# Kernel tuning notes

Hardware: AMD Instinct MI355X
Metric: run time of the kernel (lower is better)

Reference implementation:

```python
import jax, jax.numpy as jnp
import numpy as np

B, H, W = 64, 512, 512
TOP_K = 200
N_OBJS = 200
KP_THRES = 0.1
IOU_THR = 0.5
RESIZE_H, RESIZE_W = 512.0, 512.0


def setup_inputs() -> dict:
    key = jax.random.key(0)
    k1, k2, k3 = jax.random.split(key, 3)
    heatmap_y = jax.random.uniform(k1, (B, H), dtype=jnp.float32)
    heatmap_x = jax.random.uniform(k2, (B, W), dtype=jnp.float32)
    # box sizes in heatmap pixels (scaled so boxes are non-degenerate)
    size_maps = jax.random.uniform(k3, (B, H, W, 2), dtype=jnp.float32) * 64.0
    origin_shapes = jnp.full((B, 2), 1024.0, dtype=jnp.float32)
    return {"heatmap_y": heatmap_y, "heatmap_x": heatmap_x,
            "size_maps": size_maps, "origin_shapes": origin_shapes}


def _iou_one_vs_all(box, boxes):
    # box: (4,) [y1,x1,y2,x2]; boxes: (N,4)
    yy1 = jnp.maximum(box[0], boxes[:, 0])
    xx1 = jnp.maximum(box[1], boxes[:, 1])
    yy2 = jnp.minimum(box[2], boxes[:, 2])
    xx2 = jnp.minimum(box[3], boxes[:, 3])
    inter = jnp.maximum(yy2 - yy1, 0.0) * jnp.maximum(xx2 - xx1, 0.0)
    a1 = (box[2] - box[0]) * (box[3] - box[1])
    a2 = (boxes[:, 2] - boxes[:, 0]) * (boxes[:, 3] - boxes[:, 1])
    denom = a1 + a2 - inter
    return jnp.where(denom > 0.0, inter / jnp.maximum(denom, 1e-12), 0.0)


def _nms_single(boxes, scores):
    # greedy NMS over N boxes, selecting up to N_OBJS (TF combined_non_max_suppression,
    # single class, clip_boxes=False, score_threshold=-inf, zero-padded output)
    N = boxes.shape[0]

    def body(i, st):
        active, sb, ss, cnt = st
        ms = jnp.where(active, scores, -jnp.inf)
        j = jnp.argmax(ms)
        valid = ms[j] > -jnp.inf
        bj = boxes[j]
        ious = _iou_one_vs_all(bj, boxes)
        active = active & (ious <= IOU_THR)
        active = active.at[j].set(False)
        sb = sb.at[i].set(jnp.where(valid, bj, jnp.zeros_like(bj)))
        ss = ss.at[i].set(jnp.where(valid, scores[j], 0.0))
        return (active, sb, ss, cnt + valid.astype(jnp.int32))

    init = (jnp.ones((N,), dtype=bool),
            jnp.zeros((N_OBJS, 4), boxes.dtype),
            jnp.zeros((N_OBJS,), scores.dtype),
            jnp.array(0, jnp.int32))
    _, sb, ss, cnt = jax.lax.fori_loop(0, N_OBJS, body, init)
    return sb, ss, cnt


def _decode(heatmap_y, heatmap_x, size_maps, origin_shapes):
    Bd, Hd = heatmap_y.shape
    Wd = heatmap_x.shape[1]
    # rank-1 heatmap: matmul(hy[...,None], hx[...,None]^T) == outer product -> (B,H,W)
    hm = heatmap_y[:, :, None] * heatmap_x[:, None, :]
    # 3x3 max-pool peak suppression (CenterNet keep-mask)
    hmax = jax.lax.reduce_window(hm, -jnp.inf, jax.lax.max,
                                 (1, 3, 3), (1, 1, 1), 'SAME')
    hm = jnp.where(hmax == hm, hm, 0.0)
    # top-k over flattened spatial dims (c == 1)
    scores, idx = jax.lax.top_k(hm.reshape(Bd, Hd * Wd), TOP_K)  # (B,K)
    ys = idx // Wd
    xs = idx % Wd
    bidx = jnp.arange(Bd)[:, None]
    sizes = size_maps[bidx, ys, xs]                      # (B,K,2) gather_nd
    centers = jnp.stack([ys, xs], axis=-1).astype(hm.dtype)  # (B,K,2)
    tls = jnp.maximum(centers - sizes / 2.0, 0.0)        # clamp tl at 0
    brs = centers + sizes / 2.0
    br_y = jnp.minimum(brs[..., 0], RESIZE_H - 1.0)
    br_x = jnp.minimum(brs[..., 1], RESIZE_W - 1.0)
    # resize back to original image coords
    ratio = origin_shapes / jnp.asarray([RESIZE_H, RESIZE_W], dtype=hm.dtype)  # (B,2)
    ry = ratio[:, 0:1]
    rx = ratio[:, 1:2]
    boxes = jnp.stack([tls[..., 0] * ry, tls[..., 1] * rx,
                       br_y * ry, br_x * rx], axis=-1)   # (B,K,4)
    # threshold mask + scatter into -1-initialized output (indices == own positions)
    mask = scores > KP_THRES
    boxes = jnp.where(mask[..., None], boxes, -1.0)
    sc = jnp.where(mask, scores, -1.0)
    if TOP_K < N_OBJS:
        boxes = jnp.pad(boxes, ((0, 0), (0, N_OBJS - TOP_K), (0, 0)), constant_values=-1.0)
        sc = jnp.pad(sc, ((0, 0), (0, N_OBJS - TOP_K)), constant_values=-1.0)
    nb, ns, _cnt = jax.vmap(_nms_single)(boxes, sc)      # (B,N_OBJS,4), (B,N_OBJS)
    # post: -1 boxes -> inf, 0 (NMS padding) boxes -> inf
    nb = jnp.where(nb == -1.0, jnp.inf, nb)
    nb = jnp.where(nb == 0.0, jnp.inf, nb)
    classes = jnp.zeros_like(ns)                         # single class -> class id 0
    out = jnp.concatenate([nb, ns[..., None], classes[..., None]], axis=-1)
    return out.reshape(-1, N_OBJS, 6)


def reference(heatmap_y, heatmap_x, size_maps, origin_shapes):
    return _decode(heatmap_y, heatmap_x, size_maps, origin_shapes)
```

## Files before the change

### kernel.cpp

```cpp
#include <hip/hip_runtime.h>
#include <stdint.h>

#define NT 1024
#define HW 512
#define TOPK 200
#define STAIR_GEN 256
#define STAIR_T 204
#define MAXCAND 1024
#define MAXCLOSE 320

typedef unsigned long long u64;
typedef unsigned u32;

__global__ __launch_bounds__(NT) void decode_nms_kernel(
    const float* __restrict__ hyg, const float* __restrict__ hxg,
    const float* __restrict__ size_maps, const float* __restrict__ origin,
    float* __restrict__ out)
{
#pragma clang fp contract(off)
  const int b = blockIdx.x;
  const int tid = threadIdx.x;

  __shared__ float hy[HW], hx[HW];
  __shared__ int   cyI[MAXCLOSE], cxI[MAXCLOSE];
  __shared__ float cyV[MAXCLOSE], cyM[MAXCLOSE], cxV[MAXCLOSE], cxM[MAXCLOSE];
  __shared__ u64   pK[2][HW];
  __shared__ float sV[2][HW];
  __shared__ int   sI[2][HW];
  __shared__ u64   cand[MAXCAND];
  __shared__ float tS[TOPK];
  __shared__ int   tL[TOPK];
  __shared__ float4 bb4[256];
  __shared__ u64   sup[256][4];
  __shared__ int   pickL[TOPK];
  __shared__ int   nCY, nCX, nPk0, nPk1, nCand, survSh;
  __shared__ u32   Tbits;

  if (tid == 0) { nCY = 0; nCX = 0; nPk0 = 0; nPk1 = 0; nCand = 0; Tbits = 0; }
  if (tid < HW) {
    hy[tid] = hyg[(size_t)b * HW + tid];
    hx[tid] = hxg[(size_t)b * HW + tid];
  }
  __syncthreads();

  if (tid < HW) {
    int i = tid;
    float v = hy[i], m = v;
    if (i > 0)      m = fmaxf(m, hy[i - 1]);
    if (i < HW - 1) m = fmaxf(m, hy[i + 1]);
    if (v >= m * (1.0f - 1e-6f)) {
      int p = atomicAdd(&nCY, 1);
      if (p < MAXCLOSE) { cyI[p] = i; cyV[p] = v; cyM[p] = m; }
    }
    if (v == m) {
      int p = atomicAdd(&nPk0, 1);
      pK[0][p] = ((u64)__float_as_uint(v) << 32) | (u64)(0xFFFFFFFFu - (u32)i);
    }
    float w = hx[i], mw = w;
    if (i > 0)      mw = fmaxf(mw, hx[i - 1]);
    if (i < HW - 1) mw = fmaxf(mw, hx[i + 1]);
    if (w >= mw * (1.0f - 1e-6f)) {
      int p = atomicAdd(&nCX, 1);
      if (p < MAXCLOSE) { cxI[p] = i; cxV[p] = w; cxM[p] = mw; }
    }
    if (w == mw) {
      int p = atomicAdd(&nPk1, 1);
      pK[1][p] = ((u64)__float_as_uint(w) << 32) | (u64)(0xFFFFFFFFu - (u32)i);
    }
  }
  __syncthreads();

  int NP0 = nPk0, NP1 = nPk1;
  for (int d = 0; d < 2; ++d) {
    int n = d ? NP1 : NP0;
    if (tid < n) {
      u64 key = pK[d][tid];
      int rank = 0;
      #pragma unroll 8
      for (int j = 0; j < n; ++j) rank += (pK[d][j] > key) ? 1 : 0;
      sV[d][rank] = __uint_as_float((u32)(key >> 32));
      sI[d][rank] = (int)(0xFFFFFFFFu - (u32)(key & 0xFFFFFFFFu));
    }
  }
  __syncthreads();

  {
    int a = tid + 1;
    if (a <= STAIR_T && a <= NP0) {
      int bn = (STAIR_T + a - 1) / a;
      if (bn <= NP1) atomicMax(&Tbits, __float_as_uint(sV[0][a - 1] * sV[1][bn - 1]));
    }
  }
  __syncthreads();
  const float T = __uint_as_float(Tbits);

  int ncy = nCY < MAXCLOSE ? nCY : MAXCLOSE;
  int ncx = nCX < MAXCLOSE ? nCX : MAXCLOSE;
  if (tid < ncy) {
    int yi = tid;
    float vy = cyV[yi], mvy = cyM[yi];
    bool py = (vy == mvy);
    int ybase = cyI[yi] * HW;
    #pragma unroll 8
    for (int xi = 0; xi < ncx; ++xi) {
      float vx = cxV[xi], mvx = cxM[xi];
      if (py && vx == mvx) continue;
      float p = vy * vx;
      if (p == mvy * mvx && p > 0.1f && p >= T) {
        int pos = atomicAdd(&nCand, 1);
        if (pos < MAXCAND)
          cand[pos] = ((u64)__float_as_uint(p) << 32)
                    | (u64)(0xFFFFFFFFu - (u32)(ybase + cxI[xi]));
      }
    }
  }

  {
    int NY = NP0 < STAIR_GEN ? NP0 : STAIR_GEN;
    {
      int i = tid >> 6, jc = tid & 63;
      if (i < NY) {
        int jmax = STAIR_GEN / (i + 1); if (jmax > NP1) jmax = NP1;
        int jlo = jc * 4, jhi = jlo + 4; if (jhi > jmax) jhi = jmax;
        float vy = sV[0][i]; int ybase = sI[0][i] * HW;
        #pragma unroll 4
        for (int j = jlo; j < jhi; ++j) {
          float s = vy * sV[1][j];
          if (s > 0.1f && s >= T) {
            int pos = atomicAdd(&nCand, 1);
            if (pos < MAXCAND)
              cand[pos] = ((u64)__float_as_uint(s) << 32)
                        | (u64)(0xFFFFFFFFu - (u32)(ybase + sI[1][j]));
          }
        }
      }
    }
    {
      int i2 = 16 + tid;
      if (i2 < NY) {
        int jmax = STAIR_GEN / (i2 + 1); if (jmax > NP1) jmax = NP1;
        float vy = sV[0][i2]; int ybase = sI[0][i2] * HW;
        #pragma unroll 4
        for (int j = 0; j < jmax; ++j) {
          float s = vy * sV[1][j];
          if (s > 0.1f && s >= T) {
            int pos = atomicAdd(&nCand, 1);
            if (pos < MAXCAND)
              cand[pos] = ((u64)__float_as_uint(s) << 32)
                        | (u64)(0xFFFFFFFFu - (u32)(ybase + sI[1][j]));
          }
        }
      }
    }
  }
  __syncthreads();
  int C = nCand < MAXCAND ? nCand : MAXCAND;

  if (tid < C) {
    u64 k = cand[tid];
    int rank = 0;
    #pragma unroll 8
    for (int j = 0; j < C; ++j) rank += (cand[j] > k) ? 1 : 0;
    if (rank < TOPK) {
      tS[rank] = __uint_as_float((u32)(k >> 32));
      tL[rank] = (int)(0xFFFFFFFFu - (u32)(k & 0xFFFFFFFFu));
    }
  }
  __syncthreads();
  int R = C < TOPK ? C : TOPK;

  float ry = origin[b * 2 + 0] / 512.0f;
  float rx = origin[b * 2 + 1] / 512.0f;
  if (tid < 256) {
    int r = tid;
    if (r < R) {
      int lin = tL[r];
      int y = lin >> 9, x = lin & (HW - 1);
      const float* sp = size_maps + (((size_t)b * HW + y) * HW + x) * 2;
      float s0 = sp[0], s1 = sp[1];
      float cy = (float)y, cx = (float)x;
      bb4[r] = make_float4(fmaxf(cy - s0 * 0.5f, 0.0f) * ry,
                           fmaxf(cx - s1 * 0.5f, 0.0f) * rx,
                           fminf(cy + s0 * 0.5f, 511.0f) * ry,
                           fminf(cx + s1 * 0.5f, 511.0f) * rx);
    } else {
      bb4[r] = make_float4(0.f, 0.f, 0.f, 0.f);
    }
  }
  __syncthreads();

  if (tid < 256) {
    int k = tid;
    bool hasK = (k < R);
    float4 bk = bb4[k];
    float k0 = bk.x, k1 = bk.y, k2 = bk.z, k3 = bk.w;
    float a1 = (k2 - k0) * (k3 - k1);
    int wv = k >> 6;
    for (int w = 0; w < 4; ++w) {
      u64 word = 0;
      int jbase = w << 6;
      if (jbase < R && w >= wv) {
        #pragma unroll 8
        for (int jj = 0; jj < 64; ++jj) {
          int j = jbase + jj;
          float4 bj = bb4[j];
          float yy1 = fmaxf(k0, bj.x), xx1 = fmaxf(k1, bj.y);
          float yy2 = fminf(k2, bj.z), xx2 = fminf(k3, bj.w);
          float inter = fmaxf(yy2 - yy1, 0.0f) * fmaxf(xx2 - xx1, 0.0f);
          float a2 = (bj.z - bj.x) * (bj.w - bj.y);
          float denom = a1 + a2 - inter;
          float iou = (denom > 0.0f) ? (inter / fmaxf(denom, 1e-12f)) : 0.0f;
          bool s = hasK && (j > k) && (j < R) && (iou > 0.5f);
          word |= ((u64)s) << jj;
        }
      }
      sup[k][w] = word;
    }
  }
  __syncthreads();

  if (tid == 0) {
    u64 al0 = ~0ull, al1 = ~0ull, al2 = ~0ull, al3 = ~0ull;
    u64 cur[4][4], nxt[4][4];
    #pragma unroll
    for (int t = 0; t < 4; ++t) {
      cur[t][0] = sup[t][0]; cur[t][1] = sup[t][1];
      cur[t][2] = sup[t][2]; cur[t][3] = sup[t][3];
    }
    int s = 0;
    for (int k0 = 0; k0 < R; k0 += 4) {
      #pragma unroll
      for (int t = 0; t < 4; ++t) {
        nxt[t][0] = sup[k0 + 4 + t][0]; nxt[t][1] = sup[k0 + 4 + t][1];
        nxt[t][2] = sup[k0 + 4 + t][2]; nxt[t][3] = sup[k0 + 4 + t][3];
      }
      #pragma unroll
      for (int t = 0; t < 4; ++t) {
        int k = k0 + t;
        if (k < R) {
          u64 aw = (k < 64) ? al0 : (k < 128) ? al1 : (k < 192) ? al2 : al3;
          if ((aw >> (k & 63)) & 1ull) {
            pickL[s++] = k;
            al0 &= ~cur[t][0]; al1 &= ~cur[t][1];
            al2 &= ~cur[t][2]; al3 &= ~cur[t][3];
          }
        }
      }
      #pragma unroll
      for (int t = 0; t < 4; ++t) {
        cur[t][0] = nxt[t][0]; cur[t][1] = nxt[t][1];
        cur[t][2] = nxt[t][2]; cur[t][3] = nxt[t][3];
      }
    }
    survSh = s;
  }
  __syncthreads();

  int surv = survSh;
  int nNeg = TOPK - R;
  if (tid < TOPK) {
    int r = tid;
    float o0, o1, o2, o3, o4;
    if (r < surv) {
      int k = pickL[r];
      float4 bk = bb4[k];
      o0 = bk.x; o1 = bk.y; o2 = bk.z; o3 = bk.w; o4 = tS[k];
    } else if (r < surv + nNeg) {
      o0 = o1 = o2 = o3 = -1.0f; o4 = -1.0f;
    } else {
      o0 = o1 = o2 = o3 = 0.0f; o4 = 0.0f;
    }
    float* o = out + ((size_t)b * TOPK + r) * 6;
    o[0] = o0; o[1] = o1; o[2] = o2; o[3] = o3; o[4] = o4; o[5] = 0.0f;
  }
}

extern "C" void kernel_launch(void* const* d_in, const int* in_sizes, int n_in,
                              void* d_out, int out_size, void* d_ws, size_t ws_size,
                              hipStream_t stream) {
  const float* hyg = (const float*)d_in[0];
  const float* hxg = (const float*)d_in[1];
  const float* szm = (const float*)d_in[2];
  const float* org = (const float*)d_in[3];
  int B = in_sizes[0] / HW;
  decode_nms_kernel<<<dim3(B), dim3(NT), 0, stream>>>(hyg, hxg, szm, org, (float*)d_out);
}
```

Measured before the change: 253.9 us.

## Split fused decode+NMS kernel into three launches with chunked rank sorting

The single 1024-thread kernel becomes three kernels (candidate generation, top-K selection with box decode, NMS) that pass data through a per-batch workspace. Peak ranking and candidate generation now spread work over 32-wide chunks with atomic rank accumulation and bitmask-batched hits, which should balance the load better than one thread per element. The likely aim is smaller blocks with less shared memory per launch. This adds two extra launches and round trips through global memory.

```diff
diff --git a/kernel.cpp b/kernel.cpp
--- a/kernel.cpp
+++ b/kernel.cpp
@@ -1,46 +1,42 @@
 #include <hip/hip_runtime.h>
 #include <stdint.h>
 
-#define NT 1024
 #define HW 512
 #define TOPK 200
 #define STAIR_GEN 256
 #define STAIR_T 204
 #define MAXCAND 1024
 #define MAXCLOSE 320
+#define WS_STRIDE 16384
 
 typedef unsigned long long u64;
 typedef unsigned u32;
 
-__global__ __launch_bounds__(NT) void decode_nms_kernel(
+__device__ __forceinline__ u64*    wsCand(char* ws, int b){ return (u64*)(ws + (size_t)b*WS_STRIDE); }
+__device__ __forceinline__ float4* wsBB  (char* ws, int b){ return (float4*)(ws + (size_t)b*WS_STRIDE + 8192); }
+__device__ __forceinline__ float*  wsTS  (char* ws, int b){ return (float*)(ws + (size_t)b*WS_STRIDE + 12288); }
+__device__ __forceinline__ int*    wsHdr (char* ws, int b){ return (int*)(ws + (size_t)b*WS_STRIDE + 13184); }
+
+__global__ __launch_bounds__(512) void k1_gen(
     const float* __restrict__ hyg, const float* __restrict__ hxg,
-    const float* __restrict__ size_maps, const float* __restrict__ origin,
-    float* __restrict__ out)
+    char* __restrict__ ws)
 {
 #pragma clang fp contract(off)
-  const int b = blockIdx.x;
-  const int tid = threadIdx.x;
-
+  const int b = blockIdx.x, tid = threadIdx.x;
   __shared__ float hy[HW], hx[HW];
-  __shared__ int   cyI[MAXCLOSE], cxI[MAXCLOSE];
-  __shared__ float cyV[MAXCLOSE], cyM[MAXCLOSE], cxV[MAXCLOSE], cxM[MAXCLOSE];
-  __shared__ u64   pK[2][HW];
+  __shared__ int   cyI[MAXCLOSE], cxI[MAXCLOSE + 32];
+  __shared__ float cyV[MAXCLOSE], cyM[MAXCLOSE];
+  __shared__ float cxV[MAXCLOSE + 32], cxM[MAXCLOSE + 32];
+  __shared__ u64   pK[2][HW + 32];
   __shared__ float sV[2][HW];
   __shared__ int   sI[2][HW];
+  __shared__ int   rnk[2][HW];
   __shared__ u64   cand[MAXCAND];
-  __shared__ float tS[TOPK];
-  __shared__ int   tL[TOPK];
-  __shared__ float4 bb4[256];
-  __shared__ u64   sup[256][4];
-  __shared__ int   pickL[TOPK];
-  __shared__ int   nCY, nCX, nPk0, nPk1, nCand, survSh;
+  __shared__ int   nCY, nCX, nPk0, nPk1, nCand;
   __shared__ u32   Tbits;
 
   if (tid == 0) { nCY = 0; nCX = 0; nPk0 = 0; nPk1 = 0; nCand = 0; Tbits = 0; }
-  if (tid < HW) {
-    hy[tid] = hyg[(size_t)b * HW + tid];
-    hx[tid] = hxg[(size_t)b * HW + tid];
-  }
+  if (tid < HW) { hy[tid] = hyg[(size_t)b * HW + tid]; hx[tid] = hxg[(size_t)b * HW + tid]; }
   __syncthreads();
 
   if (tid < HW) {
@@ -70,17 +66,44 @@
   }
   __syncthreads();
 
-  int NP0 = nPk0, NP1 = nPk1;
-  for (int d = 0; d < 2; ++d) {
-    int n = d ? NP1 : NP0;
-    if (tid < n) {
-      u64 key = pK[d][tid];
-      int rank = 0;
-      #pragma unroll 8
-      for (int j = 0; j < n; ++j) rank += (pK[d][j] > key) ? 1 : 0;
-      sV[d][rank] = __uint_as_float((u32)(key >> 32));
-      sI[d][rank] = (int)(0xFFFFFFFFu - (u32)(key & 0xFFFFFFFFu));
-    }
+  const int NP0 = nPk0, NP1 = nPk1;
+  const int ncy = nCY < MAXCLOSE ? nCY : MAXCLOSE;
+  const int ncx = nCX < MAXCLOSE ? nCX : MAXCLOSE;
+  const int np0 = (NP0 + 31) & ~31, np1 = (NP1 + 31) & ~31;
+  const int ncxp = (ncx + 31) & ~31;
+  for (int k = NP0 + tid; k < np0; k += 512) pK[0][k] = 0;
+  for (int k = NP1 + tid; k < np1; k += 512) pK[1][k] = 0;
+  for (int k = ncx + tid; k < ncxp; k += 512) { cxV[k] = 0.f; cxM[k] = 0.f; }
+  if (tid < NP0) rnk[0][tid] = 0;
+  if (tid < NP1) rnk[1][tid] = 0;
+  __syncthreads();
+
+  {
+    const int nch0 = np0 >> 5, nch1 = np1 >> 5;
+    const int U0 = NP0 * nch0, U1 = NP1 * nch1, U = U0 + U1;
+    for (int u = tid; u < U; u += 512) {
+      int d = (u >= U0);
+      int v = d ? (u - U0) : u;
+      int nch = d ? nch1 : nch0;
+      int i = v / nch, c = v - i * nch;
+      u64 key = pK[d][i];
+      const u64* row = &pK[d][c << 5];
+      int r = 0;
+      #pragma unroll
+      for (int jj = 0; jj < 32; ++jj) r += (row[jj] > key) ? 1 : 0;
+      if (r) atomicAdd(&rnk[d][i], r);
+    }
+  }
+  __syncthreads();
+  if (tid < NP0) {
+    u64 key = pK[0][tid]; int r = rnk[0][tid];
+    sV[0][r] = __uint_as_float((u32)(key >> 32));
+    sI[0][r] = (int)(0xFFFFFFFFu - (u32)(key & 0xFFFFFFFFu));
+  }
+  if (tid < NP1) {
+    u64 key = pK[1][tid]; int r = rnk[1][tid];
+    sV[1][r] = __uint_as_float((u32)(key >> 32));
+    sI[1][r] = (int)(0xFFFFFFFFu - (u32)(key & 0xFFFFFFFFu));
   }
   __syncthreads();
 
@@ -94,36 +117,46 @@
   __syncthreads();
   const float T = __uint_as_float(Tbits);
 
-  int ncy = nCY < MAXCLOSE ? nCY : MAXCLOSE;
-  int ncx = nCX < MAXCLOSE ? nCX : MAXCLOSE;
-  if (tid < ncy) {
-    int yi = tid;
-    float vy = cyV[yi], mvy = cyM[yi];
-    bool py = (vy == mvy);
-    int ybase = cyI[yi] * HW;
-    #pragma unroll 8
-    for (int xi = 0; xi < ncx; ++xi) {
-      float vx = cxV[xi], mvx = cxM[xi];
-      if (py && vx == mvx) continue;
-      float p = vy * vx;
-      if (p == mvy * mvx && p > 0.1f && p >= T) {
-        int pos = atomicAdd(&nCand, 1);
-        if (pos < MAXCAND)
-          cand[pos] = ((u64)__float_as_uint(p) << 32)
-                    | (u64)(0xFFFFFFFFu - (u32)(ybase + cxI[xi]));
+  {
+    const int nchx = ncxp >> 5;
+    const int U = ncy * nchx;
+    for (int u = tid; u < U; u += 512) {
+      int yi = u / nchx, c = u - yi * nchx;
+      float vy = cyV[yi], mvy = cyM[yi];
+      bool py = (vy == mvy);
+      int ybase = cyI[yi] * HW, xb = c << 5;
+      for (int j8 = 0; j8 < 32; j8 += 8) {
+        unsigned hits = 0;
+        #pragma unroll
+        for (int q = 0; q < 8; ++q) {
+          int xi = xb + j8 + q;
+          float vx = cxV[xi], mvx = cxM[xi];
+          float pr = vy * vx;
+          bool h = (!(py && vx == mvx)) && (pr == mvy * mvx) && (pr > 0.1f) && (pr >= T);
+          hits |= ((unsigned)h) << q;
+        }
+        if (__builtin_expect(hits != 0, 0)) {
+          for (int q = 0; q < 8; ++q) if ((hits >> q) & 1u) {
+            int xi = xb + j8 + q;
+            float pr = vy * cxV[xi];
+            int pos = atomicAdd(&nCand, 1);
+            if (pos < MAXCAND)
+              cand[pos] = ((u64)__float_as_uint(pr) << 32)
+                        | (u64)(0xFFFFFFFFu - (u32)(ybase + cxI[xi]));
+          }
+        }
       }
     }
   }
 
   {
     int NY = NP0 < STAIR_GEN ? NP0 : STAIR_GEN;
-    {
-      int i = tid >> 6, jc = tid & 63;
+    if (tid < 256) {
+      int i = tid >> 4, jc = tid & 15;
       if (i < NY) {
         int jmax = STAIR_GEN / (i + 1); if (jmax > NP1) jmax = NP1;
-        int jlo = jc * 4, jhi = jlo + 4; if (jhi > jmax) jhi = jmax;
+        int jlo = jc * 16, jhi = jlo + 16; if (jhi > jmax) jhi = jmax;
         float vy = sV[0][i]; int ybase = sI[0][i] * HW;
-        #pragma unroll 4
         for (int j = jlo; j < jhi; ++j) {
           float s = vy * sV[1][j];
           if (s > 0.1f && s >= T) {
@@ -134,13 +167,11 @@
           }
         }
       }
-    }
-    {
-      int i2 = 16 + tid;
+    } else {
+      int i2 = tid - 240;
       if (i2 < NY) {
         int jmax = STAIR_GEN / (i2 + 1); if (jmax > NP1) jmax = NP1;
         float vy = sV[0][i2]; int ybase = sI[0][i2] * HW;
-        #pragma unroll 4
         for (int j = 0; j < jmax; ++j) {
           float s = vy * sV[1][j];
           if (s > 0.1f && s >= T) {
@@ -155,41 +186,81 @@
   }
   __syncthreads();
   int C = nCand < MAXCAND ? nCand : MAXCAND;
-
-  if (tid < C) {
-    u64 k = cand[tid];
+  u64* cg = wsCand(ws, b);
+  for (int i = tid; i < C; i += 512) cg[i] = cand[i];
+  if (tid == 0) wsHdr(ws, b)[0] = C;
+}
+
+__global__ __launch_bounds__(512) void k2_select(
+    const float* __restrict__ size_maps, const float* __restrict__ origin,
+    char* __restrict__ ws)
+{
+#pragma clang fp contract(off)
+  const int b = blockIdx.x, tid = threadIdx.x;
+  __shared__ u64 cand[MAXCAND];
+  __shared__ float tS[TOPK];
+  __shared__ int   tL[TOPK];
+  const int C = wsHdr(ws, b)[0];
+  const int C8 = (C + 7) & ~7;
+  u64* cg = wsCand(ws, b);
+  for (int i = tid; i < C; i += 512) cand[i] = cg[i];
+  for (int i = C + tid; i < C8; i += 512) cand[i] = 0;
+  __syncthreads();
+
+  for (int i = tid; i < C; i += 512) {
+    u64 k = cand[i];
     int rank = 0;
-    #pragma unroll 8
-    for (int j = 0; j < C; ++j) rank += (cand[j] > k) ? 1 : 0;
+    for (int j = 0; j < C8; j += 8) {
+      #pragma unroll
+      for (int q = 0; q < 8; ++q) rank += (cand[j + q] > k) ? 1 : 0;
+    }
     if (rank < TOPK) {
       tS[rank] = __uint_as_float((u32)(k >> 32));
       tL[rank] = (int)(0xFFFFFFFFu - (u32)(k & 0xFFFFFFFFu));
     }
   }
   __syncthreads();
-  int R = C < TOPK ? C : TOPK;
+  const int R = C < TOPK ? C : TOPK;
 
   float ry = origin[b * 2 + 0] / 512.0f;
   float rx = origin[b * 2 + 1] / 512.0f;
+  float4* bbG = wsBB(ws, b);
+  float*  tsG = wsTS(ws, b);
   if (tid < 256) {
-    int r = tid;
-    if (r < R) {
-      int lin = tL[r];
+    float4 v = make_float4(0.f, 0.f, 0.f, 0.f);
+    if (tid < R) {
+      int lin = tL[tid];
       int y = lin >> 9, x = lin & (HW - 1);
       const float* sp = size_maps + (((size_t)b * HW + y) * HW + x) * 2;
       float s0 = sp[0], s1 = sp[1];
       float cy = (float)y, cx = (float)x;
-      bb4[r] = make_float4(fmaxf(cy - s0 * 0.5f, 0.0f) * ry,
-                           fmaxf(cx - s1 * 0.5f, 0.0f) * rx,
-                           fminf(cy + s0 * 0.5f, 511.0f) * ry,
-                           fminf(cx + s1 * 0.5f, 511.0f) * rx);
-    } else {
-      bb4[r] = make_float4(0.f, 0.f, 0.f, 0.f);
-    }
-  }
-  __syncthreads();
-
-  if (tid < 256) {
+      v = make_float4(fmaxf(cy - s0 * 0.5f, 0.0f) * ry,
+                      fmaxf(cx - s1 * 0.5f, 0.0f) * rx,
+                      fminf(cy + s0 * 0.5f, 511.0f) * ry,
+                      fminf(cx + s1 * 0.5f, 511.0f) * rx);
+    }
+    bbG[tid] = v;
+    if (tid < TOPK) tsG[tid] = (tid < R) ? tS[tid] : 0.f;
+  }
+}
+
+__global__ __launch_bounds__(256) void k3_nms(
+    char* __restrict__ ws, float* __restrict__ out)
+{
+#pragma clang fp contract(off)
+  const int b = blockIdx.x, tid = threadIdx.x;
+  __shared__ float4 bb4[256];
+  __shared__ float  tS[TOPK];
+  __shared__ u64    sup[256][4];
+  __shared__ int    pickL[TOPK];
+  __shared__ int    survSh;
+  const int C = wsHdr(ws, b)[0];
+  const int R = C < TOPK ? C : TOPK;
+  bb4[tid] = wsBB(ws, b)[tid];
+  if (tid < TOPK) tS[tid] = wsTS(ws, b)[tid];
+  __syncthreads();
+
+  {
     int k = tid;
     bool hasK = (k < R);
     float4 bk = bb4[k];
@@ -283,5 +354,8 @@
   const float* szm = (const float*)d_in[2];
   const float* org = (const float*)d_in[3];
   int B = in_sizes[0] / HW;
-  decode_nms_kernel<<<dim3(B), dim3(NT), 0, stream>>>(hyg, hxg, szm, org, (float*)d_out);
+  char* ws = (char*)d_ws;
+  k1_gen<<<dim3(B), dim3(512), 0, stream>>>(hyg, hxg, ws);
+  k2_select<<<dim3(B), dim3(512), 0, stream>>>(szm, org, ws);
+  k3_nms<<<dim3(B), dim3(256), 0, stream>>>(ws, (float*)d_out);
 }
```

New measurement: 260.7 us. 1.03x slower.

## Replace shared atomics with ballot/scan compaction and halve block size

Applied to the files above, without the earlier changes.

Peak and close-candidate compaction now uses wave ballots with per-wave prefix counts instead of shared atomicAdd, and the staircase candidates are counted first and then scattered through a prefix scan. The threshold is reduced with shuffles instead of atomicMax. The block shrinks from 1024 to 512 threads, and the coincidence loop is batched in groups of eight to cut branching. The aim is to remove atomic contention and serialization, at the cost of extra passes and barriers and fewer threads for the rank sorts.

```diff
diff --git a/kernel.cpp b/kernel.cpp
--- a/kernel.cpp
+++ b/kernel.cpp
@@ -1,7 +1,7 @@
 #include <hip/hip_runtime.h>
 #include <stdint.h>
 
-#define NT 1024
+#define NT 512
 #define HW 512
 #define TOPK 200
 #define STAIR_GEN 256
@@ -18,174 +18,251 @@
     float* __restrict__ out)
 {
 #pragma clang fp contract(off)
-  const int b = blockIdx.x;
-  const int tid = threadIdx.x;
+  const int b = blockIdx.x, tid = threadIdx.x;
+  const int lid = tid & 63, wid = tid >> 6;
 
   __shared__ float hy[HW], hx[HW];
-  __shared__ int   cyI[MAXCLOSE], cxI[MAXCLOSE];
-  __shared__ float cyV[MAXCLOSE], cyM[MAXCLOSE], cxV[MAXCLOSE], cxM[MAXCLOSE];
+  __shared__ int   cyI[MAXCLOSE], cxI[MAXCLOSE + 8];
+  __shared__ float cyV[MAXCLOSE], cyM[MAXCLOSE];
+  __shared__ float cxV[MAXCLOSE + 8], cxM[MAXCLOSE + 8];
   __shared__ u64   pK[2][HW];
   __shared__ float sV[2][HW];
   __shared__ int   sI[2][HW];
-  __shared__ u64   cand[MAXCAND];
+  __shared__ int   wcnt[4][8];
+  __shared__ float tred[8];
+  __shared__ int   cCnt[256], rowBase[256];
+  __shared__ int   wscan[4];
+  __shared__ u64   cand[MAXCAND + 8];
   __shared__ float tS[TOPK];
   __shared__ int   tL[TOPK];
   __shared__ float4 bb4[256];
   __shared__ u64   sup[256][4];
   __shared__ int   pickL[TOPK];
-  __shared__ int   nCY, nCX, nPk0, nPk1, nCand, survSh;
-  __shared__ u32   Tbits;
-
-  if (tid == 0) { nCY = 0; nCX = 0; nPk0 = 0; nPk1 = 0; nCand = 0; Tbits = 0; }
-  if (tid < HW) {
-    hy[tid] = hyg[(size_t)b * HW + tid];
-    hx[tid] = hxg[(size_t)b * HW + tid];
-  }
-  __syncthreads();
-
-  if (tid < HW) {
+  __shared__ int   nCoin, survSh, Ssh;
+  __shared__ float Tsh;
+
+  if (tid == 0) nCoin = 0;
+  hy[tid] = hyg[(size_t)b * HW + tid];
+  hx[tid] = hxg[(size_t)b * HW + tid];
+  __syncthreads();
+
+  {
     int i = tid;
     float v = hy[i], m = v;
     if (i > 0)      m = fmaxf(m, hy[i - 1]);
     if (i < HW - 1) m = fmaxf(m, hy[i + 1]);
-    if (v >= m * (1.0f - 1e-6f)) {
-      int p = atomicAdd(&nCY, 1);
-      if (p < MAXCLOSE) { cyI[p] = i; cyV[p] = v; cyM[p] = m; }
-    }
-    if (v == m) {
-      int p = atomicAdd(&nPk0, 1);
-      pK[0][p] = ((u64)__float_as_uint(v) << 32) | (u64)(0xFFFFFFFFu - (u32)i);
-    }
     float w = hx[i], mw = w;
     if (i > 0)      mw = fmaxf(mw, hx[i - 1]);
     if (i < HW - 1) mw = fmaxf(mw, hx[i + 1]);
-    if (w >= mw * (1.0f - 1e-6f)) {
-      int p = atomicAdd(&nCX, 1);
-      if (p < MAXCLOSE) { cxI[p] = i; cxV[p] = w; cxM[p] = mw; }
-    }
-    if (w == mw) {
-      int p = atomicAdd(&nPk1, 1);
-      pK[1][p] = ((u64)__float_as_uint(w) << 32) | (u64)(0xFFFFFFFFu - (u32)i);
-    }
-  }
-  __syncthreads();
-
-  int NP0 = nPk0, NP1 = nPk1;
-  for (int d = 0; d < 2; ++d) {
+    bool cY = (v >= m  * (1.0f - 1e-6f));
+    bool pY = (v == m);
+    bool cX = (w >= mw * (1.0f - 1e-6f));
+    bool pX = (w == mw);
+    u64 mCY = __ballot(cY), mPY = __ballot(pY);
+    u64 mCX = __ballot(cX), mPX = __ballot(pX);
+    if (lid == 0) {
+      wcnt[0][wid] = (int)__popcll(mCY); wcnt[1][wid] = (int)__popcll(mPY);
+      wcnt[2][wid] = (int)__popcll(mCX); wcnt[3][wid] = (int)__popcll(mPX);
+    }
+    __syncthreads();
+    int b0 = 0, b1 = 0, b2 = 0, b3 = 0;
+    for (int q = 0; q < wid; ++q) {
+      b0 += wcnt[0][q]; b1 += wcnt[1][q]; b2 += wcnt[2][q]; b3 += wcnt[3][q];
+    }
+    u64 ltm = (1ull << lid) - 1;
+    if (cY) { int p = b0 + (int)__popcll(mCY & ltm);
+      if (p < MAXCLOSE) { cyI[p] = i; cyV[p] = v; cyM[p] = m; } }
+    if (pY) { int p = b1 + (int)__popcll(mPY & ltm);
+      pK[0][p] = ((u64)__float_as_uint(v) << 32) | (u64)(0xFFFFFFFFu - (u32)i); }
+    if (cX) { int p = b2 + (int)__popcll(mCX & ltm);
+      if (p < MAXCLOSE) { cxI[p] = i; cxV[p] = w; cxM[p] = mw; } }
+    if (pX) { int p = b3 + (int)__popcll(mPX & ltm);
+      pK[1][p] = ((u64)__float_as_uint(w) << 32) | (u64)(0xFFFFFFFFu - (u32)i); }
+  }
+  __syncthreads();
+
+  int nCY = 0, nPk0 = 0, nCX = 0, nPk1 = 0;
+  for (int q = 0; q < 8; ++q) {
+    nCY += wcnt[0][q]; nPk0 += wcnt[1][q]; nCX += wcnt[2][q]; nPk1 += wcnt[3][q];
+  }
+  const int NP0 = nPk0, NP1 = nPk1;
+  const int ncy = nCY < MAXCLOSE ? nCY : MAXCLOSE;
+  const int ncx = nCX < MAXCLOSE ? nCX : MAXCLOSE;
+  const int ncx8 = (ncx + 7) & ~7;
+  if (tid < ncx8 - ncx) { cxV[ncx + tid] = 0.f; cxM[ncx + tid] = 0.f; }
+  __syncthreads();
+
+  if (NP0 <= 256 && NP1 <= 256) {
+    int d = tid >> 8, i = tid & 255;
     int n = d ? NP1 : NP0;
-    if (tid < n) {
-      u64 key = pK[d][tid];
+    if (i < n) {
+      u64 key = pK[d][i];
       int rank = 0;
       #pragma unroll 8
       for (int j = 0; j < n; ++j) rank += (pK[d][j] > key) ? 1 : 0;
       sV[d][rank] = __uint_as_float((u32)(key >> 32));
       sI[d][rank] = (int)(0xFFFFFFFFu - (u32)(key & 0xFFFFFFFFu));
     }
+  } else {
+    for (int d = 0; d < 2; ++d) {
+      int n = d ? NP1 : NP0;
+      for (int i = tid; i < n; i += NT) {
+        u64 key = pK[d][i];
+        int rank = 0;
+        for (int j = 0; j < n; ++j) rank += (pK[d][j] > key) ? 1 : 0;
+        sV[d][rank] = __uint_as_float((u32)(key >> 32));
+        sI[d][rank] = (int)(0xFFFFFFFFu - (u32)(key & 0xFFFFFFFFu));
+      }
+    }
   }
   __syncthreads();
 
   {
+    float t = 0.f;
     int a = tid + 1;
     if (a <= STAIR_T && a <= NP0) {
       int bn = (STAIR_T + a - 1) / a;
-      if (bn <= NP1) atomicMax(&Tbits, __float_as_uint(sV[0][a - 1] * sV[1][bn - 1]));
-    }
-  }
-  __syncthreads();
-  const float T = __uint_as_float(Tbits);
-
-  int ncy = nCY < MAXCLOSE ? nCY : MAXCLOSE;
-  int ncx = nCX < MAXCLOSE ? nCX : MAXCLOSE;
+      if (bn <= NP1) t = sV[0][a - 1] * sV[1][bn - 1];
+    }
+    for (int o = 32; o; o >>= 1) t = fmaxf(t, __shfl_xor(t, o));
+    if (lid == 0) tred[wid] = t;
+    __syncthreads();
+    if (tid == 0) {
+      float m = tred[0];
+      for (int q = 1; q < 8; ++q) m = fmaxf(m, tred[q]);
+      Tsh = m;
+    }
+    __syncthreads();
+  }
+  const float T = Tsh;
+
+  const int NY = NP0 < STAIR_GEN ? NP0 : STAIR_GEN;
+  if (tid < 256) {
+    int c = 0;
+    if (tid < NY) {
+      int jmax = STAIR_GEN / (tid + 1); if (jmax > NP1) jmax = NP1;
+      float vy = sV[0][tid];
+      #pragma unroll 8
+      for (int j = 0; j < jmax; ++j) {
+        float s = vy * sV[1][j];
+        c += (s > 0.1f && s >= T) ? 1 : 0;
+      }
+    }
+    cCnt[tid] = c;
+  }
+  __syncthreads();
+
+  {
+    int x = (tid < 256) ? cCnt[tid] : 0;
+    int orig = x;
+    for (int o = 1; o < 64; o <<= 1) {
+      int y = __shfl_up(x, o);
+      if (lid >= o) x += y;
+    }
+    if (lid == 63 && wid < 4) wscan[wid] = x;
+    __syncthreads();
+    if (tid < 256) {
+      int base = 0;
+      for (int q = 0; q < wid; ++q) base += wscan[q];
+      rowBase[tid] = base + x - orig;
+    }
+    if (tid == 0) Ssh = wscan[0] + wscan[1] + wscan[2] + wscan[3];
+    __syncthreads();
+  }
+  const int S = Ssh < MAXCAND ? Ssh : MAXCAND;
+
+  if (tid < 256) {
+    int i = tid >> 4, jc = tid & 15;
+    if (i < NY) {
+      int ci = cCnt[i], rb = rowBase[i];
+      float vy = sV[0][i]; int ybase = sI[0][i] * HW;
+      int jlo = jc * 16, jhi = jlo + 16; if (jhi > ci) jhi = ci;
+      for (int j = jlo; j < jhi; ++j) {
+        int slot = rb + j;
+        if (slot < MAXCAND)
+          cand[slot] = ((u64)__float_as_uint(vy * sV[1][j]) << 32)
+                     | (u64)(0xFFFFFFFFu - (u32)(ybase + sI[1][j]));
+      }
+    }
+  } else {
+    int i2 = tid - 240;
+    if (i2 < NY) {
+      int ci = cCnt[i2], rb = rowBase[i2];
+      float vy = sV[0][i2]; int ybase = sI[0][i2] * HW;
+      for (int j = 0; j < ci; ++j) {
+        int slot = rb + j;
+        if (slot < MAXCAND)
+          cand[slot] = ((u64)__float_as_uint(vy * sV[1][j]) << 32)
+                     | (u64)(0xFFFFFFFFu - (u32)(ybase + sI[1][j]));
+      }
+    }
+  }
+
   if (tid < ncy) {
-    int yi = tid;
-    float vy = cyV[yi], mvy = cyM[yi];
+    float vy = cyV[tid], mvy = cyM[tid];
     bool py = (vy == mvy);
-    int ybase = cyI[yi] * HW;
-    #pragma unroll 8
-    for (int xi = 0; xi < ncx; ++xi) {
-      float vx = cxV[xi], mvx = cxM[xi];
-      if (py && vx == mvx) continue;
-      float p = vy * vx;
-      if (p == mvy * mvx && p > 0.1f && p >= T) {
-        int pos = atomicAdd(&nCand, 1);
-        if (pos < MAXCAND)
-          cand[pos] = ((u64)__float_as_uint(p) << 32)
-                    | (u64)(0xFFFFFFFFu - (u32)(ybase + cxI[xi]));
-      }
-    }
-  }
-
-  {
-    int NY = NP0 < STAIR_GEN ? NP0 : STAIR_GEN;
-    {
-      int i = tid >> 6, jc = tid & 63;
-      if (i < NY) {
-        int jmax = STAIR_GEN / (i + 1); if (jmax > NP1) jmax = NP1;
-        int jlo = jc * 4, jhi = jlo + 4; if (jhi > jmax) jhi = jmax;
-        float vy = sV[0][i]; int ybase = sI[0][i] * HW;
-        #pragma unroll 4
-        for (int j = jlo; j < jhi; ++j) {
-          float s = vy * sV[1][j];
-          if (s > 0.1f && s >= T) {
-            int pos = atomicAdd(&nCand, 1);
-            if (pos < MAXCAND)
-              cand[pos] = ((u64)__float_as_uint(s) << 32)
-                        | (u64)(0xFFFFFFFFu - (u32)(ybase + sI[1][j]));
-          }
+    int ybase = cyI[tid] * HW;
+    for (int xb = 0; xb < ncx8; xb += 8) {
+      unsigned hits = 0;
+      #pragma unroll
+      for (int q = 0; q < 8; ++q) {
+        int xi = xb + q;
+        float vx = cxV[xi], mvx = cxM[xi];
+        float pr = vy * vx;
+        bool h = (!(py && vx == mvx)) && (pr == mvy * mvx)
+               && (pr > 0.1f) && (pr >= T);
+        hits |= ((unsigned)h) << q;
+      }
+      if (__builtin_expect(hits != 0, 0)) {
+        for (int q = 0; q < 8; ++q) if ((hits >> q) & 1u) {
+          int xi = xb + q;
+          float pr = vy * cxV[xi];
+          int pos = atomicAdd(&nCoin, 1);
+          int slot = S + pos;
+          if (slot < MAXCAND)
+            cand[slot] = ((u64)__float_as_uint(pr) << 32)
+                       | (u64)(0xFFFFFFFFu - (u32)(ybase + cxI[xi]));
         }
       }
     }
-    {
-      int i2 = 16 + tid;
-      if (i2 < NY) {
-        int jmax = STAIR_GEN / (i2 + 1); if (jmax > NP1) jmax = NP1;
-        float vy = sV[0][i2]; int ybase = sI[0][i2] * HW;
-        #pragma unroll 4
-        for (int j = 0; j < jmax; ++j) {
-          float s = vy * sV[1][j];
-          if (s > 0.1f && s >= T) {
-            int pos = atomicAdd(&nCand, 1);
-            if (pos < MAXCAND)
-              cand[pos] = ((u64)__float_as_uint(s) << 32)
-                        | (u64)(0xFFFFFFFFu - (u32)(ybase + sI[1][j]));
-          }
-        }
-      }
-    }
-  }
-  __syncthreads();
-  int C = nCand < MAXCAND ? nCand : MAXCAND;
-
-  if (tid < C) {
-    u64 k = cand[tid];
+  }
+  __syncthreads();
+  int C = S + nCoin; if (C > MAXCAND) C = MAXCAND;
+  const int C8 = (C + 7) & ~7;
+  if (tid < C8 - C) cand[C + tid] = 0;
+  __syncthreads();
+
+  for (int i = tid; i < C; i += NT) {
+    u64 k = cand[i];
     int rank = 0;
-    #pragma unroll 8
-    for (int j = 0; j < C; ++j) rank += (cand[j] > k) ? 1 : 0;
+    for (int j = 0; j < C8; j += 8) {
+      #pragma unroll
+      for (int q = 0; q < 8; ++q) rank += (cand[j + q] > k) ? 1 : 0;
+    }
     if (rank < TOPK) {
       tS[rank] = __uint_as_float((u32)(k >> 32));
       tL[rank] = (int)(0xFFFFFFFFu - (u32)(k & 0xFFFFFFFFu));
     }
   }
   __syncthreads();
-  int R = C < TOPK ? C : TOPK;
+  const int R = C < TOPK ? C : TOPK;
 
   float ry = origin[b * 2 + 0] / 512.0f;
   float rx = origin[b * 2 + 1] / 512.0f;
   if (tid < 256) {
-    int r = tid;
-    if (r < R) {
-      int lin = tL[r];
+    float4 v = make_float4(0.f, 0.f, 0.f, 0.f);
+    if (tid < R) {
+      int lin = tL[tid];
       int y = lin >> 9, x = lin & (HW - 1);
       const float* sp = size_maps + (((size_t)b * HW + y) * HW + x) * 2;
       float s0 = sp[0], s1 = sp[1];
       float cy = (float)y, cx = (float)x;
-      bb4[r] = make_float4(fmaxf(cy - s0 * 0.5f, 0.0f) * ry,
-                           fmaxf(cx - s1 * 0.5f, 0.0f) * rx,
-                           fminf(cy + s0 * 0.5f, 511.0f) * ry,
-                           fminf(cx + s1 * 0.5f, 511.0f) * rx);
-    } else {
-      bb4[r] = make_float4(0.f, 0.f, 0.f, 0.f);
-    }
+      v = make_float4(fmaxf(cy - s0 * 0.5f, 0.0f) * ry,
+                      fmaxf(cx - s1 * 0.5f, 0.0f) * rx,
+                      fminf(cy + s0 * 0.5f, 511.0f) * ry,
+                      fminf(cx + s1 * 0.5f, 511.0f) * rx);
+    }
+    bb4[tid] = v;
   }
   __syncthreads();
 
```

After: 258.3 us. No clear change (+1.7%).
